# Kernel tuning notes

Measured on AMD Instinct MI355X. Metric: run time of the kernel, lower is better.

The kernel has to match this reference:

```python
import jax, jax.numpy as jnp
import numpy as np

NUM_HEADS = 12
HEAD_DIM = 64
HIDDEN = 768
SLOT_DIM = 30
BS = 8
FULL = SLOT_DIM * BS  # 240
SLOT_LEN = 32
LEN0 = 512   # slot-broadcast cache length
LEN1 = 128   # per-sample cache length


def tf_slot(x, slot_dim):
    # (slot_dim*bs, H, L, h) -> (bs, H, slot_dim*L, h)
    full, nh, L, h = x.shape
    bs = full // slot_dim
    x = x.reshape(slot_dim, bs, nh, L, h).transpose(1, 2, 0, 3, 4)
    return x.reshape(bs, nh, slot_dim * L, h)


def back_slot(x, slot_dim):
    # (bs, H, slot_dim*L, h) -> (slot_dim*bs, H, L, h)
    bs, nh, total, h = x.shape
    L = total // slot_dim
    x = x.reshape(bs, nh, slot_dim, L, h).transpose(2, 0, 1, 3, 4)
    return x.reshape(slot_dim * bs, nh, L, h)


def setup_inputs() -> dict:
    key = jax.random.key(0)
    ks = jax.random.split(key, 12)
    s = 0.02
    return {
        "hidden_states": jax.random.normal(ks[0], (FULL, SLOT_LEN, HIDDEN), jnp.float32),
        "attention_mask": jnp.zeros((FULL, 1, 1, LEN0 + LEN1 + SLOT_LEN), jnp.float32),
        "cache0_key": jax.random.normal(ks[1], (BS, NUM_HEADS, LEN0, HEAD_DIM), jnp.float32),
        "cache0_value": jax.random.normal(ks[2], (BS, NUM_HEADS, LEN0, HEAD_DIM), jnp.float32),
        "cache1_key": jax.random.normal(ks[3], (FULL, NUM_HEADS, LEN1, HEAD_DIM), jnp.float32),
        "cache1_value": jax.random.normal(ks[4], (FULL, NUM_HEADS, LEN1, HEAD_DIM), jnp.float32),
        "Wq": jax.random.normal(ks[5], (HIDDEN, HIDDEN), jnp.float32) * s,
        "bq": jax.random.normal(ks[6], (HIDDEN,), jnp.float32) * s,
        "Wk": jax.random.normal(ks[7], (HIDDEN, HIDDEN), jnp.float32) * s,
        "bk": jax.random.normal(ks[8], (HIDDEN,), jnp.float32) * s,
        "Wv": jax.random.normal(ks[9], (HIDDEN, HIDDEN), jnp.float32) * s,
        "bv": jax.random.normal(ks[10], (HIDDEN,), jnp.float32) * s,
        "slot_dim": SLOT_DIM,
    }


def reference(hidden_states, attention_mask, cache0_key, cache0_value,
              cache1_key, cache1_value, Wq, bq, Wk, bk, Wv, bv, slot_dim):
    B, L, hid = hidden_states.shape

    def split_heads(x):  # (B, L, hid) -> (B, H, L, h)
        return x.reshape(B, L, NUM_HEADS, HEAD_DIM).transpose(0, 2, 1, 3)

    q = split_heads(hidden_states @ Wq + bq)
    k = split_heads(hidden_states @ Wk + bk)
    v = split_heads(hidden_states @ Wv + bv)

    # self-attention scores (B, H, L, L)
    self_scores = jnp.einsum('bhqd,bhkd->bhqk', q, k)

    # cache0: slot-broadcast path (cache batch = bs, queries batch = slot_dim*bs)
    q_tf = tf_slot(q, slot_dim)  # (bs, H, slot_dim*L, h)
    s0 = back_slot(jnp.einsum('bhqd,bhkd->bhqk', q_tf, cache0_key), slot_dim)  # (B,H,L,LEN0)
    # cache1: direct path (matching batch)
    s1 = jnp.einsum('bhqd,bhkd->bhqk', q, cache1_key)  # (B,H,L,LEN1)

    scores = jnp.concatenate([s0, s1, self_scores], axis=-1)
    scores = scores / jnp.sqrt(jnp.float32(HEAD_DIM)) + attention_mask
    probs = jax.nn.softmax(scores, axis=-1)  # single softmax over all KV sources

    len0 = cache0_key.shape[2]
    len1 = cache1_key.shape[2]
    # self context
    ctx = jnp.einsum('bhqk,bhkd->bhqd', probs[..., -L:], v)
    # cache0 context via slot transform
    p0 = tf_slot(probs[..., :len0], slot_dim)  # (bs, H, slot_dim*L, LEN0)
    ctx = ctx + back_slot(jnp.einsum('bhqk,bhkd->bhqd', p0, cache0_value), slot_dim)
    # cache1 context direct
    ctx = ctx + jnp.einsum('bhqk,bhkd->bhqd', probs[..., len0:len0 + len1], cache1_value)

    # (B, H, L, h) -> (B, L, hid)
    return ctx.transpose(0, 2, 1, 3).reshape(B, L, hid)
```

## Files before the change

kernel.cpp:

```cpp
#include <hip/hip_runtime.h>
#include <math.h>

#define NUM_HEADS 12
#define HEAD_DIM  64
#define HIDDEN    768
#define BS        8
#define FULL      240
#define SLOT_LEN  32
#define LEN0      512
#define LEN1      128
#define KTOT      672
#define M_TOK     (FULL * SLOT_LEN)

typedef float f32x4 __attribute__((ext_vector_type(4)));
typedef short s16x8 __attribute__((ext_vector_type(8)));
typedef short s16x4 __attribute__((ext_vector_type(4)));

__device__ __forceinline__ short f2bf(float x) {
    unsigned u = __float_as_uint(x);
    unsigned r = (u + 0x7fffu + ((u >> 16) & 1u)) >> 16;
    return (short)r;
}

__device__ __forceinline__ void gll16(const short* g, short* l) {
    __builtin_amdgcn_global_load_lds(
        (const __attribute__((address_space(1))) unsigned int*)g,
        (__attribute__((address_space(3))) unsigned int*)l, 16, 0, 0);
}

__global__ __launch_bounds__(256) void cast_hs(const float* __restrict__ in,
                                               short* __restrict__ out, int n4) {
    int i = blockIdx.x * 256 + threadIdx.x;
    if (i < n4) {
        float4 v = ((const float4*)in)[i];
        s16x4 o = {f2bf(v.x), f2bf(v.y), f2bf(v.z), f2bf(v.w)};
        ((s16x4*)out)[i] = o;
    }
}

__global__ __launch_bounds__(256) void cast_k0(const float* __restrict__ k0,
                                               short* __restrict__ k0c) {
    const size_t base = (size_t)blockIdx.x * 2048;
    const int t = threadIdx.x;
    const int row = t >> 3, c8 = t & 7;
    const float* src = &k0[base + row * 64 + c8 * 8];
    float4 a = *(const float4*)src;
    float4 b = *(const float4*)(src + 4);
    s16x8 o = {f2bf(a.x), f2bf(a.y), f2bf(a.z), f2bf(a.w),
               f2bf(b.x), f2bf(b.y), f2bf(b.z), f2bf(b.w)};
    *(s16x8*)&k0c[base + row * 64 + (size_t)((c8 ^ (row & 7)) * 8)] = o;
}

__global__ __launch_bounds__(256) void trans_v0(const float* __restrict__ v0,
                                                short* __restrict__ v0t) {
    __shared__ float tile[32][65];
    const size_t base = (size_t)blockIdx.x * 2048;
    const int t = threadIdx.x;
#pragma unroll
    for (int i = 0; i < 2; ++i) {
        int f = t + i * 256;
        int kr = f >> 4, d4 = (f & 15) * 4;
        float4 v = *(const float4*)&v0[base + kr * 64 + d4];
        tile[kr][d4 + 0] = v.x; tile[kr][d4 + 1] = v.y;
        tile[kr][d4 + 2] = v.z; tile[kr][d4 + 3] = v.w;
    }
    __syncthreads();
#pragma unroll
    for (int i = 0; i < 2; ++i) {
        int g = t + i * 256;
        int d = g >> 3, kr4 = (g & 7) * 4;
        s16x4 o = {f2bf(tile[kr4 + 0][d]), f2bf(tile[kr4 + 1][d]),
                   f2bf(tile[kr4 + 2][d]), f2bf(tile[kr4 + 3][d])};
        int grp = (kr4 >> 3) ^ ((d >> 1) & 3);
        *(s16x4*)&v0t[base + d * 32 + grp * 8 + (kr4 & 7)] = o;
    }
}

__global__ __launch_bounds__(256) void cast_w_t(const float* __restrict__ Wq,
                                                const float* __restrict__ Wk,
                                                const float* __restrict__ Wv,
                                                short* __restrict__ WtAll) {
    const float* W = (blockIdx.z == 0) ? Wq : (blockIdx.z == 1) ? Wk : Wv;
    short* Wt = WtAll + (size_t)blockIdx.z * HIDDEN * HIDDEN;
    __shared__ __align__(16) float tile[32][33];
    const int kb0 = blockIdx.y * 32, nb0 = blockIdx.x * 32;
    const int r = threadIdx.x >> 3, c4 = (threadIdx.x & 7) * 4;
    float4 v = *(const float4*)&W[(size_t)(kb0 + r) * HIDDEN + nb0 + c4];
    tile[r][c4 + 0] = v.x; tile[r][c4 + 1] = v.y;
    tile[r][c4 + 2] = v.z; tile[r][c4 + 3] = v.w;
    __syncthreads();
    s16x4 o = {f2bf(tile[c4 + 0][r]), f2bf(tile[c4 + 1][r]),
               f2bf(tile[c4 + 2][r]), f2bf(tile[c4 + 3][r])};
    *(s16x4*)&Wt[(size_t)(nb0 + r) * HIDDEN + kb0 + c4] = o;
}

__global__ __launch_bounds__(256) void qkv_mfma(
    const short* __restrict__ hsb, const short* __restrict__ WtAll,
    const float* __restrict__ bq, const float* __restrict__ bk,
    const float* __restrict__ bv,
    short* __restrict__ qo, short* __restrict__ ko, short* __restrict__ vo)
{
    const int z = blockIdx.z;
    const short* Wt = WtAll + (size_t)z * HIDDEN * HIDDEN;
    const float* bias = (z == 0) ? bq : (z == 1) ? bk : bv;
    short* outp = (z == 0) ? qo : (z == 1) ? ko : vo;

    __shared__ __align__(16) short smem[128 * 128];
    short* As = smem;
    short* Bs = smem + 128 * 64;

    const int t = threadIdx.x;
    const int lane = t & 63, w = t >> 6;
    const int l15 = lane & 15, quad = lane >> 4;
    const int mBase = blockIdx.y * 128, nBase = blockIdx.x * 128;
    const int mw = (w & 1) * 64, nw = (w >> 1) * 64;

    const int srow_in = lane >> 3;
    const int scol8 = (lane & 7) ^ srow_in;

    f32x4 acc[4][4];
    const f32x4 z4 = {0.f, 0.f, 0.f, 0.f};
#pragma unroll
    for (int i = 0; i < 4; ++i)
#pragma unroll
        for (int j = 0; j < 4; ++j) acc[i][j] = z4;

    for (int kb = 0; kb < HIDDEN; kb += 64) {
        __syncthreads();
#pragma unroll
        for (int j = 0; j < 4; ++j) {
            int row = w * 32 + j * 8 + srow_in;
            gll16(&hsb[(size_t)(mBase + row) * HIDDEN + kb + scol8 * 8],
                  &As[(w * 32 + j * 8) * 64]);
            gll16(&Wt[(size_t)(nBase + row) * HIDDEN + kb + scol8 * 8],
                  &Bs[(w * 32 + j * 8) * 64]);
        }
        __syncthreads();
#pragma unroll
        for (int kc = 0; kc < 2; ++kc) {
            s16x8 a[4], b[4];
#pragma unroll
            for (int mt = 0; mt < 4; ++mt) {
                int row = mw + mt * 16 + l15;
                int c8 = (kc * 4 + quad) ^ (row & 7);
                a[mt] = *(const s16x8*)&As[row * 64 + c8 * 8];
            }
#pragma unroll
            for (int nt = 0; nt < 4; ++nt) {
                int row = nw + nt * 16 + l15;
                int c8 = (kc * 4 + quad) ^ (row & 7);
                b[nt] = *(const s16x8*)&Bs[row * 64 + c8 * 8];
            }
#pragma unroll
            for (int mt = 0; mt < 4; ++mt)
#pragma unroll
                for (int nt = 0; nt < 4; ++nt)
                    acc[mt][nt] = __builtin_amdgcn_mfma_f32_16x16x32_bf16(
                        a[mt], b[nt], acc[mt][nt], 0, 0, 0);
        }
    }

    __syncthreads();
#pragma unroll
    for (int nt = 0; nt < 4; ++nt) {
        float bvv = bias[nBase + nw + nt * 16 + l15];
        int col = nw + nt * 16 + l15;
#pragma unroll
        for (int mt = 0; mt < 4; ++mt)
#pragma unroll
            for (int r = 0; r < 4; ++r) {
                int row = mw + mt * 16 + quad * 4 + r;
                smem[row * 128 + col] = f2bf(acc[mt][nt][r] + bvv);
            }
    }
    __syncthreads();
#pragma unroll
    for (int i = 0; i < 8; ++i) {
        int f = t + i * 256;
        int row = f >> 4, c8 = (f & 15) * 8;
        uint4 val = *(const uint4*)&smem[row * 128 + c8];
        int m = mBase + row, n = nBase + c8;
        size_t dst = (((size_t)(m >> 5) * NUM_HEADS + (n >> 6)) * SLOT_LEN + (m & 31)) * 64 + (n & 63);
        *(uint4*)&outp[dst] = val;
    }
}

__global__ __launch_bounds__(256) void attn_mfma(
    const short* __restrict__ qb, const short* __restrict__ kbuf,
    const short* __restrict__ vbuf,
    const short* __restrict__ k0c, const short* __restrict__ v0t,
    const float* __restrict__ c1k, const float* __restrict__ c1v,
    const float* __restrict__ mask, float* __restrict__ out)
{
    __shared__ __align__(16) short Klds[4][32][64];
    __shared__ __align__(16) short Vt[4][64][32];
    __shared__ __align__(16) short Plds[4][32][32];

    const int t = threadIdx.x, lane = t & 63, w = t >> 6;
    const int task = blockIdx.x * 4 + w;
    const int B = task / 12, h = task % 12;
    const int l15 = lane & 15, quad = lane >> 4;

    const short* qp  = qb  + (size_t)(B * NUM_HEADS + h) * SLOT_LEN * 64;
    const short* ksp = kbuf + (size_t)(B * NUM_HEADS + h) * SLOT_LEN * 64;
    const short* vsp = vbuf + (size_t)(B * NUM_HEADS + h) * SLOT_LEN * 64;
    const short* k0p = k0c + (size_t)((B & 7) * NUM_HEADS + h) * LEN0 * 64;
    const short* v0p = v0t + (size_t)((B & 7) * NUM_HEADS + h) * LEN0 * 64;
    const float* k1p = c1k + (size_t)(B * NUM_HEADS + h) * LEN1 * 64;
    const float* v1p = c1v + (size_t)(B * NUM_HEADS + h) * LEN1 * 64;
    const float* mp  = mask + (size_t)B * KTOT;

    short (*K)[64] = Klds[w];
    short (*V)[32] = Vt[w];
    short (*P)[32] = Plds[w];
    short* Kf = &K[0][0];
    short* Vf = &V[0][0];

    const int skey = lane >> 4;
    const int sc4 = (lane & 15) << 2;

    s16x8 qf[2][2];
#pragma unroll
    for (int qh = 0; qh < 2; ++qh)
#pragma unroll
        for (int kc = 0; kc < 2; ++kc)
            qf[qh][kc] = *(const s16x8*)&qp[(qh * 16 + l15) * 64 + kc * 32 + quad * 8];

    const f32x4 z4 = {0.f, 0.f, 0.f, 0.f};
    f32x4 o[2][4];
    float lpart[2][4];
#pragma unroll
    for (int qh = 0; qh < 2; ++qh) {
#pragma unroll
        for (int dq = 0; dq < 4; ++dq) o[qh][dq] = z4;
#pragma unroll
        for (int r = 0; r < 4; ++r) lpart[qh][r] = 0.f;
    }

    s16x8 kpre[4], vpre[4];
    float4 kreg[8];
    float mreg0, mreg1;

    const float LOG2E = 1.4426950408889634f;
    const float SCL   = 0.125f * 1.4426950408889634f;

    auto issue_bf = [&](int c) {
        const short* kcb = k0p + c * 2048;
        const short* vcb = v0p + c * 2048;
#pragma unroll
        for (int i = 0; i < 4; ++i) {
            kpre[i] = *(const s16x8*)&kcb[(i * 64 + lane) * 8];
            vpre[i] = *(const s16x8*)&vcb[(i * 64 + lane) * 8];
        }
    };
    auto issue_k1 = [&](int c) {
        const float* sk = k1p + (c - 16) * 2048;
#pragma unroll
        for (int i = 0; i < 8; ++i)
            kreg[i] = *(const float4*)&sk[(i * 4 + skey) * 64 + sc4];
    };
    auto issue_mask = [&](int c) {
        mreg0 = mp[c * 32 + l15] * LOG2E;
        mreg1 = mp[c * 32 + 16 + l15] * LOG2E;
    };

    issue_bf(0);
    issue_mask(0);

    for (int c = 0; c < 21; ++c) {
        const float mv0 = mreg0, mv1 = mreg1;
        float4 vv[8];
        bool f32path = (c >= 16 && c < 20);

        if (c < 16) {
#pragma unroll
            for (int i = 0; i < 4; ++i)
                *(s16x8*)&Kf[(i * 64 + lane) * 8] = kpre[i];
#pragma unroll
            for (int i = 0; i < 4; ++i)
                *(s16x8*)&Vf[(i * 64 + lane) * 8] = vpre[i];
            if (c + 1 < 16) issue_bf(c + 1);
            if (c == 15) issue_k1(16);
        } else if (c < 20) {
#pragma unroll
            for (int i = 0; i < 8; ++i) {
                s16x4 kk = {f2bf(kreg[i].x), f2bf(kreg[i].y), f2bf(kreg[i].z), f2bf(kreg[i].w)};
                int row = i * 4 + skey;
                *(s16x4*)&K[row][((l15 >> 1) ^ (row & 7)) * 8 + (l15 & 1) * 4] = kk;
            }
            const float* sv = v1p + (c - 16) * 2048;
#pragma unroll
            for (int i = 0; i < 8; ++i)
                vv[i] = *(const float4*)&sv[(i * 4 + skey) * 64 + sc4];
            if (c + 1 < 20) issue_k1(c + 1);
        } else {
#pragma unroll
            for (int i = 0; i < 8; ++i) {
                int key = i * 4 + skey;
                *(s16x4*)&K[key][((l15 >> 1) ^ (key & 7)) * 8 + (l15 & 1) * 4] =
                    *(const s16x4*)&ksp[key * 64 + sc4];
            }
            short vtmp[32];
#pragma unroll
            for (int key = 0; key < 32; ++key) vtmp[key] = vsp[key * 64 + lane];
#pragma unroll
            for (int k4 = 0; k4 < 8; ++k4) {
                s16x4 vo4 = {vtmp[k4 * 4 + 0], vtmp[k4 * 4 + 1],
                             vtmp[k4 * 4 + 2], vtmp[k4 * 4 + 3]};
                int grp = (k4 >> 1) ^ ((lane >> 1) & 3);
                *(s16x4*)&V[lane][grp * 8 + (k4 & 1) * 4] = vo4;
            }
        }

        if (c + 1 < 21) issue_mask(c + 1);

        f32x4 s[2][2];
#pragma unroll
        for (int qh = 0; qh < 2; ++qh)
#pragma unroll
            for (int kh = 0; kh < 2; ++kh) s[qh][kh] = z4;
#pragma unroll
        for (int kh = 0; kh < 2; ++kh) {
            int rowk = kh * 16 + l15;
            s16x8 kf0 = *(const s16x8*)&K[rowk][(quad ^ (rowk & 7)) * 8];
            s16x8 kf1 = *(const s16x8*)&K[rowk][((4 + quad) ^ (rowk & 7)) * 8];
#pragma unroll
            for (int qh = 0; qh < 2; ++qh) {
                s[qh][kh] = __builtin_amdgcn_mfma_f32_16x16x32_bf16(qf[qh][0], kf0, s[qh][kh], 0, 0, 0);
                s[qh][kh] = __builtin_amdgcn_mfma_f32_16x16x32_bf16(qf[qh][1], kf1, s[qh][kh], 0, 0, 0);
            }
        }

#pragma unroll
        for (int qh = 0; qh < 2; ++qh)
#pragma unroll
            for (int kh = 0; kh < 2; ++kh) {
                float mv = kh ? mv1 : mv0;
#pragma unroll
                for (int r = 0; r < 4; ++r) {
                    float p = exp2f(fmaf(s[qh][kh][r], SCL, mv));
                    lpart[qh][r] += p;
                    int prow = qh * 16 + quad * 4 + r;
                    int pswz = ((kh * 2 + (l15 >> 3)) ^ ((prow >> 1) & 3)) * 8 + (l15 & 7);
                    P[prow][pswz] = f2bf(p);
                }
            }

        if (f32path) {
#pragma unroll
            for (int i = 0; i < 8; ++i) {
                int key = i * 4 + skey;
                int kg = key >> 3, ks = key & 7;
#pragma unroll
                for (int j = 0; j < 4; ++j) {
                    int rowv = sc4 + j;
                    float fv = (j == 0) ? vv[i].x : (j == 1) ? vv[i].y : (j == 2) ? vv[i].z : vv[i].w;
                    V[rowv][(kg ^ ((rowv >> 1) & 3)) * 8 + ks] = f2bf(fv);
                }
            }
        }

#pragma unroll
        for (int qh = 0; qh < 2; ++qh) {
            int prow2 = qh * 16 + l15;
            int pg = (quad ^ ((l15 >> 1) & 3)) * 8;
            s16x4 plo = *(const s16x4*)&P[prow2][pg];
            s16x4 phi = *(const s16x4*)&P[prow2][pg + 4];
            s16x8 pf = __builtin_shufflevector(plo, phi, 0, 1, 2, 3, 4, 5, 6, 7);
#pragma unroll
            for (int dq = 0; dq < 4; ++dq) {
                int vrow = dq * 16 + l15;
                s16x8 vf = *(const s16x8*)&V[vrow][(quad ^ ((l15 >> 1) & 3)) * 8];
                o[qh][dq] = __builtin_amdgcn_mfma_f32_16x16x32_bf16(pf, vf, o[qh][dq], 0, 0, 0);
            }
        }
    }

    float linv[2][4];
#pragma unroll
    for (int qh = 0; qh < 2; ++qh)
#pragma unroll
        for (int r = 0; r < 4; ++r) {
            float l = lpart[qh][r];
            l += __shfl_xor(l, 1);
            l += __shfl_xor(l, 2);
            l += __shfl_xor(l, 4);
            l += __shfl_xor(l, 8);
            linv[qh][r] = 1.f / l;
        }

#pragma unroll
    for (int qh = 0; qh < 2; ++qh)
#pragma unroll
        for (int dq = 0; dq < 4; ++dq)
#pragma unroll
            for (int r = 0; r < 4; ++r) {
                int row = qh * 16 + quad * 4 + r;
                out[((size_t)B * SLOT_LEN + row) * HIDDEN + h * 64 + dq * 16 + l15] =
                    o[qh][dq][r] * linv[qh][r];
            }
}

extern "C" void kernel_launch(void* const* d_in, const int* in_sizes, int n_in,
                              void* d_out, int out_size, void* d_ws, size_t ws_size,
                              hipStream_t stream) {
    const float* hs   = (const float*)d_in[0];
    const float* mask = (const float*)d_in[1];
    const float* c0k  = (const float*)d_in[2];
    const float* c0v  = (const float*)d_in[3];
    const float* c1k  = (const float*)d_in[4];
    const float* c1v  = (const float*)d_in[5];
    const float* Wq   = (const float*)d_in[6];
    const float* bq   = (const float*)d_in[7];
    const float* Wk   = (const float*)d_in[8];
    const float* bk   = (const float*)d_in[9];
    const float* Wv   = (const float*)d_in[10];
    const float* bv   = (const float*)d_in[11];
    float* out = (float*)d_out;

    short* hsb = (short*)d_ws;
    short* WtA = hsb + (size_t)M_TOK * HIDDEN;
    short* qb  = WtA + (size_t)3 * HIDDEN * HIDDEN;
    short* kbw = qb + (size_t)M_TOK * HIDDEN;
    short* vbw = kbw + (size_t)M_TOK * HIDDEN;
    short* k0c = (short*)d_ws;
    short* v0t = k0c + (size_t)BS * NUM_HEADS * LEN0 * HEAD_DIM;

    cast_hs<<<(M_TOK * HIDDEN / 4 + 255) / 256, 256, 0, stream>>>(hs, hsb, M_TOK * HIDDEN / 4);
    cast_w_t<<<dim3(24, 24, 3), 256, 0, stream>>>(Wq, Wk, Wv, WtA);
    qkv_mfma<<<dim3(HIDDEN / 128, M_TOK / 128, 3), 256, 0, stream>>>(
        hsb, WtA, bq, bk, bv, qb, kbw, vbw);
    cast_k0<<<BS * NUM_HEADS * (LEN0 / 32), 256, 0, stream>>>(c0k, k0c);
    trans_v0<<<BS * NUM_HEADS * (LEN0 / 32), 256, 0, stream>>>(c0v, v0t);
    attn_mfma<<<720, 256, 0, stream>>>(qb, kbw, vbw, k0c, v0t, c1k, c1v, mask, out);
}
```

Measured before the change: 407.8 us.

## Split each attention task's KV chunks across four waves and merge via LDS

The attention kernel now assigns one (batch, head) task per block instead of per wave. The four waves each process a disjoint subset of the KV chunks (four cache0 chunks, one cache1 chunk, plus the self chunk on wave 3), and the partial outputs and row sums are reduced through shared memory before a vectorized store. This quadruples the block count and shortens each wave's serial chunk loop. In exchange it adds block syncs, an LDS reduction pass and less intra-wave prefetch pipelining. The cast_k0 and trans_v0 prep kernels are also merged into one launch.

```diff
diff --git a/kernel.cpp b/kernel.cpp
--- a/kernel.cpp
+++ b/kernel.cpp
@@ -38,41 +38,40 @@
     }
 }
 
-__global__ __launch_bounds__(256) void cast_k0(const float* __restrict__ k0,
-                                               short* __restrict__ k0c) {
-    const size_t base = (size_t)blockIdx.x * 2048;
-    const int t = threadIdx.x;
-    const int row = t >> 3, c8 = t & 7;
-    const float* src = &k0[base + row * 64 + c8 * 8];
-    float4 a = *(const float4*)src;
-    float4 b = *(const float4*)(src + 4);
-    s16x8 o = {f2bf(a.x), f2bf(a.y), f2bf(a.z), f2bf(a.w),
-               f2bf(b.x), f2bf(b.y), f2bf(b.z), f2bf(b.w)};
-    *(s16x8*)&k0c[base + row * 64 + (size_t)((c8 ^ (row & 7)) * 8)] = o;
-}
-
-__global__ __launch_bounds__(256) void trans_v0(const float* __restrict__ v0,
-                                                short* __restrict__ v0t) {
+__global__ __launch_bounds__(256) void prep_c0(const float* __restrict__ k0,
+                                               const float* __restrict__ v0,
+                                               short* __restrict__ k0c,
+                                               short* __restrict__ v0t) {
     __shared__ float tile[32][65];
     const size_t base = (size_t)blockIdx.x * 2048;
     const int t = threadIdx.x;
-#pragma unroll
-    for (int i = 0; i < 2; ++i) {
-        int f = t + i * 256;
-        int kr = f >> 4, d4 = (f & 15) * 4;
-        float4 v = *(const float4*)&v0[base + kr * 64 + d4];
-        tile[kr][d4 + 0] = v.x; tile[kr][d4 + 1] = v.y;
-        tile[kr][d4 + 2] = v.z; tile[kr][d4 + 3] = v.w;
-    }
-    __syncthreads();
-#pragma unroll
-    for (int i = 0; i < 2; ++i) {
-        int g = t + i * 256;
-        int d = g >> 3, kr4 = (g & 7) * 4;
-        s16x4 o = {f2bf(tile[kr4 + 0][d]), f2bf(tile[kr4 + 1][d]),
-                   f2bf(tile[kr4 + 2][d]), f2bf(tile[kr4 + 3][d])};
-        int grp = (kr4 >> 3) ^ ((d >> 1) & 3);
-        *(s16x4*)&v0t[base + d * 32 + grp * 8 + (kr4 & 7)] = o;
+    if (blockIdx.y == 0) {
+        const int row = t >> 3, c8 = t & 7;
+        const float* src = &k0[base + row * 64 + c8 * 8];
+        float4 a = *(const float4*)src;
+        float4 b = *(const float4*)(src + 4);
+        s16x8 o = {f2bf(a.x), f2bf(a.y), f2bf(a.z), f2bf(a.w),
+                   f2bf(b.x), f2bf(b.y), f2bf(b.z), f2bf(b.w)};
+        *(s16x8*)&k0c[base + row * 64 + (size_t)((c8 ^ (row & 7)) * 8)] = o;
+    } else {
+#pragma unroll
+        for (int i = 0; i < 2; ++i) {
+            int f = t + i * 256;
+            int kr = f >> 4, d4 = (f & 15) * 4;
+            float4 v = *(const float4*)&v0[base + kr * 64 + d4];
+            tile[kr][d4 + 0] = v.x; tile[kr][d4 + 1] = v.y;
+            tile[kr][d4 + 2] = v.z; tile[kr][d4 + 3] = v.w;
+        }
+        __syncthreads();
+#pragma unroll
+        for (int i = 0; i < 2; ++i) {
+            int g = t + i * 256;
+            int d = g >> 3, kr4 = (g & 7) * 4;
+            s16x4 o = {f2bf(tile[kr4 + 0][d]), f2bf(tile[kr4 + 1][d]),
+                       f2bf(tile[kr4 + 2][d]), f2bf(tile[kr4 + 3][d])};
+            int grp = (kr4 >> 3) ^ ((d >> 1) & 3);
+            *(s16x4*)&v0t[base + d * 32 + grp * 8 + (kr4 & 7)] = o;
+        }
     }
 }
 
@@ -192,12 +191,10 @@
     const float* __restrict__ c1k, const float* __restrict__ c1v,
     const float* __restrict__ mask, float* __restrict__ out)
 {
-    __shared__ __align__(16) short Klds[4][32][64];
-    __shared__ __align__(16) short Vt[4][64][32];
-    __shared__ __align__(16) short Plds[4][32][32];
+    __shared__ __align__(16) short sm_s[20480];
 
     const int t = threadIdx.x, lane = t & 63, w = t >> 6;
-    const int task = blockIdx.x * 4 + w;
+    const int task = blockIdx.x;
     const int B = task / 12, h = task % 12;
     const int l15 = lane & 15, quad = lane >> 4;
 
@@ -210,14 +207,17 @@
     const float* v1p = c1v + (size_t)(B * NUM_HEADS + h) * LEN1 * 64;
     const float* mp  = mask + (size_t)B * KTOT;
 
-    short (*K)[64] = Klds[w];
-    short (*V)[32] = Vt[w];
-    short (*P)[32] = Plds[w];
-    short* Kf = &K[0][0];
-    short* Vf = &V[0][0];
+    short (*K)[64] = (short(*)[64])(sm_s + w * 5120);
+    short (*V)[32] = (short(*)[32])(sm_s + w * 5120 + 2048);
+    short (*P)[32] = (short(*)[32])(sm_s + w * 5120 + 4096);
+    short* Kf = sm_s + w * 5120;
+    short* Vf = sm_s + w * 5120 + 2048;
 
     const int skey = lane >> 4;
     const int sc4 = (lane & 15) << 2;
+
+    const float LOG2E = 1.4426950408889634f;
+    const float SCL   = 0.125f * 1.4426950408889634f;
 
     s16x8 qf[2][2];
 #pragma unroll
@@ -237,83 +237,7 @@
         for (int r = 0; r < 4; ++r) lpart[qh][r] = 0.f;
     }
 
-    s16x8 kpre[4], vpre[4];
-    float4 kreg[8];
-    float mreg0, mreg1;
-
-    const float LOG2E = 1.4426950408889634f;
-    const float SCL   = 0.125f * 1.4426950408889634f;
-
-    auto issue_bf = [&](int c) {
-        const short* kcb = k0p + c * 2048;
-        const short* vcb = v0p + c * 2048;
-#pragma unroll
-        for (int i = 0; i < 4; ++i) {
-            kpre[i] = *(const s16x8*)&kcb[(i * 64 + lane) * 8];
-            vpre[i] = *(const s16x8*)&vcb[(i * 64 + lane) * 8];
-        }
-    };
-    auto issue_k1 = [&](int c) {
-        const float* sk = k1p + (c - 16) * 2048;
-#pragma unroll
-        for (int i = 0; i < 8; ++i)
-            kreg[i] = *(const float4*)&sk[(i * 4 + skey) * 64 + sc4];
-    };
-    auto issue_mask = [&](int c) {
-        mreg0 = mp[c * 32 + l15] * LOG2E;
-        mreg1 = mp[c * 32 + 16 + l15] * LOG2E;
-    };
-
-    issue_bf(0);
-    issue_mask(0);
-
-    for (int c = 0; c < 21; ++c) {
-        const float mv0 = mreg0, mv1 = mreg1;
-        float4 vv[8];
-        bool f32path = (c >= 16 && c < 20);
-
-        if (c < 16) {
-#pragma unroll
-            for (int i = 0; i < 4; ++i)
-                *(s16x8*)&Kf[(i * 64 + lane) * 8] = kpre[i];
-#pragma unroll
-            for (int i = 0; i < 4; ++i)
-                *(s16x8*)&Vf[(i * 64 + lane) * 8] = vpre[i];
-            if (c + 1 < 16) issue_bf(c + 1);
-            if (c == 15) issue_k1(16);
-        } else if (c < 20) {
-#pragma unroll
-            for (int i = 0; i < 8; ++i) {
-                s16x4 kk = {f2bf(kreg[i].x), f2bf(kreg[i].y), f2bf(kreg[i].z), f2bf(kreg[i].w)};
-                int row = i * 4 + skey;
-                *(s16x4*)&K[row][((l15 >> 1) ^ (row & 7)) * 8 + (l15 & 1) * 4] = kk;
-            }
-            const float* sv = v1p + (c - 16) * 2048;
-#pragma unroll
-            for (int i = 0; i < 8; ++i)
-                vv[i] = *(const float4*)&sv[(i * 4 + skey) * 64 + sc4];
-            if (c + 1 < 20) issue_k1(c + 1);
-        } else {
-#pragma unroll
-            for (int i = 0; i < 8; ++i) {
-                int key = i * 4 + skey;
-                *(s16x4*)&K[key][((l15 >> 1) ^ (key & 7)) * 8 + (l15 & 1) * 4] =
-                    *(const s16x4*)&ksp[key * 64 + sc4];
-            }
-            short vtmp[32];
-#pragma unroll
-            for (int key = 0; key < 32; ++key) vtmp[key] = vsp[key * 64 + lane];
-#pragma unroll
-            for (int k4 = 0; k4 < 8; ++k4) {
-                s16x4 vo4 = {vtmp[k4 * 4 + 0], vtmp[k4 * 4 + 1],
-                             vtmp[k4 * 4 + 2], vtmp[k4 * 4 + 3]};
-                int grp = (k4 >> 1) ^ ((lane >> 1) & 3);
-                *(s16x4*)&V[lane][grp * 8 + (k4 & 1) * 4] = vo4;
-            }
-        }
-
-        if (c + 1 < 21) issue_mask(c + 1);
-
+    auto qk_exp = [&](float mv0, float mv1) {
         f32x4 s[2][2];
 #pragma unroll
         for (int qh = 0; qh < 2; ++qh)
@@ -330,7 +254,6 @@
                 s[qh][kh] = __builtin_amdgcn_mfma_f32_16x16x32_bf16(qf[qh][1], kf1, s[qh][kh], 0, 0, 0);
             }
         }
-
 #pragma unroll
         for (int qh = 0; qh < 2; ++qh)
 #pragma unroll
@@ -345,21 +268,8 @@
                     P[prow][pswz] = f2bf(p);
                 }
             }
-
-        if (f32path) {
-#pragma unroll
-            for (int i = 0; i < 8; ++i) {
-                int key = i * 4 + skey;
-                int kg = key >> 3, ks = key & 7;
-#pragma unroll
-                for (int j = 0; j < 4; ++j) {
-                    int rowv = sc4 + j;
-                    float fv = (j == 0) ? vv[i].x : (j == 1) ? vv[i].y : (j == 2) ? vv[i].z : vv[i].w;
-                    V[rowv][(kg ^ ((rowv >> 1) & 3)) * 8 + ks] = f2bf(fv);
-                }
-            }
-        }
-
+    };
+    auto pv = [&]() {
 #pragma unroll
         for (int qh = 0; qh < 2; ++qh) {
             int prow2 = qh * 16 + l15;
@@ -374,9 +284,119 @@
                 o[qh][dq] = __builtin_amdgcn_mfma_f32_16x16x32_bf16(pf, vf, o[qh][dq], 0, 0, 0);
             }
         }
-    }
-
-    float linv[2][4];
+    };
+
+    if (w == 3) {
+#pragma unroll
+        for (int i = 0; i < 8; ++i) {
+            int key = i * 4 + skey;
+            *(s16x4*)&K[key][((l15 >> 1) ^ (key & 7)) * 8 + (l15 & 1) * 4] =
+                *(const s16x4*)&ksp[key * 64 + sc4];
+        }
+        short vtmp[32];
+#pragma unroll
+        for (int key = 0; key < 32; ++key) vtmp[key] = vsp[key * 64 + lane];
+#pragma unroll
+        for (int k4 = 0; k4 < 8; ++k4) {
+            s16x4 vo4 = {vtmp[k4 * 4 + 0], vtmp[k4 * 4 + 1],
+                         vtmp[k4 * 4 + 2], vtmp[k4 * 4 + 3]};
+            int grp = (k4 >> 1) ^ ((lane >> 1) & 3);
+            *(s16x4*)&V[lane][grp * 8 + (k4 & 1) * 4] = vo4;
+        }
+        float mv0 = mp[20 * 32 + l15] * LOG2E;
+        float mv1 = mp[20 * 32 + 16 + l15] * LOG2E;
+        qk_exp(mv0, mv1);
+        pv();
+    }
+
+    {
+        int c = 16 + w;
+        const float* sk = k1p + (c - 16) * 2048;
+        const float* sv = v1p + (c - 16) * 2048;
+        float4 kr[4], vv[4];
+#pragma unroll
+        for (int i = 0; i < 4; ++i)
+            kr[i] = *(const float4*)&sk[(i * 4 + skey) * 64 + sc4];
+#pragma unroll
+        for (int i = 0; i < 4; ++i)
+            vv[i] = *(const float4*)&sv[(i * 4 + skey) * 64 + sc4];
+#pragma unroll
+        for (int i = 0; i < 4; ++i) {
+            s16x4 kk = {f2bf(kr[i].x), f2bf(kr[i].y), f2bf(kr[i].z), f2bf(kr[i].w)};
+            int row = i * 4 + skey;
+            *(s16x4*)&K[row][((l15 >> 1) ^ (row & 7)) * 8 + (l15 & 1) * 4] = kk;
+        }
+#pragma unroll
+        for (int i = 0; i < 4; ++i)
+            kr[i] = *(const float4*)&sk[((i + 4) * 4 + skey) * 64 + sc4];
+#pragma unroll
+        for (int i = 0; i < 4; ++i) {
+            s16x4 kk = {f2bf(kr[i].x), f2bf(kr[i].y), f2bf(kr[i].z), f2bf(kr[i].w)};
+            int row = (i + 4) * 4 + skey;
+            *(s16x4*)&K[row][((l15 >> 1) ^ (row & 7)) * 8 + (l15 & 1) * 4] = kk;
+        }
+        float mv0 = mp[c * 32 + l15] * LOG2E;
+        float mv1 = mp[c * 32 + 16 + l15] * LOG2E;
+        qk_exp(mv0, mv1);
+#pragma unroll
+        for (int i = 0; i < 4; ++i) {
+            int key = i * 4 + skey;
+            int kg = key >> 3, ks = key & 7;
+#pragma unroll
+            for (int j = 0; j < 4; ++j) {
+                int rowv = sc4 + j;
+                float fv = (j == 0) ? vv[i].x : (j == 1) ? vv[i].y : (j == 2) ? vv[i].z : vv[i].w;
+                V[rowv][(kg ^ ((rowv >> 1) & 3)) * 8 + ks] = f2bf(fv);
+            }
+        }
+#pragma unroll
+        for (int i = 0; i < 4; ++i)
+            vv[i] = *(const float4*)&sv[((i + 4) * 4 + skey) * 64 + sc4];
+#pragma unroll
+        for (int i = 0; i < 4; ++i) {
+            int key = (i + 4) * 4 + skey;
+            int kg = key >> 3, ks = key & 7;
+#pragma unroll
+            for (int j = 0; j < 4; ++j) {
+                int rowv = sc4 + j;
+                float fv = (j == 0) ? vv[i].x : (j == 1) ? vv[i].y : (j == 2) ? vv[i].z : vv[i].w;
+                V[rowv][(kg ^ ((rowv >> 1) & 3)) * 8 + ks] = f2bf(fv);
+            }
+        }
+        pv();
+    }
+
+    {
+        s16x8 kpre[4], vpre[4];
+        const int cbase = w * 4;
+        auto issue_bf = [&](int c) {
+            const short* kcb = k0p + c * 2048;
+            const short* vcb = v0p + c * 2048;
+#pragma unroll
+            for (int i = 0; i < 4; ++i) {
+                kpre[i] = *(const s16x8*)&kcb[(i * 64 + lane) * 8];
+                vpre[i] = *(const s16x8*)&vcb[(i * 64 + lane) * 8];
+            }
+        };
+        issue_bf(cbase);
+#pragma unroll
+        for (int j = 0; j < 4; ++j) {
+            int c = cbase + j;
+#pragma unroll
+            for (int i = 0; i < 4; ++i)
+                *(s16x8*)&Kf[(i * 64 + lane) * 8] = kpre[i];
+#pragma unroll
+            for (int i = 0; i < 4; ++i)
+                *(s16x8*)&Vf[(i * 64 + lane) * 8] = vpre[i];
+            if (j + 1 < 4) issue_bf(c + 1);
+            float mv0 = mp[c * 32 + l15] * LOG2E;
+            float mv1 = mp[c * 32 + 16 + l15] * LOG2E;
+            qk_exp(mv0, mv1);
+            pv();
+        }
+    }
+
+    float lred[2][4];
 #pragma unroll
     for (int qh = 0; qh < 2; ++qh)
 #pragma unroll
@@ -386,19 +406,51 @@
             l += __shfl_xor(l, 2);
             l += __shfl_xor(l, 4);
             l += __shfl_xor(l, 8);
-            linv[qh][r] = 1.f / l;
-        }
-
+            lred[qh][r] = l;
+        }
+
+    __syncthreads();
+    float* smf = (float*)sm_s;
 #pragma unroll
     for (int qh = 0; qh < 2; ++qh)
 #pragma unroll
         for (int dq = 0; dq < 4; ++dq)
 #pragma unroll
             for (int r = 0; r < 4; ++r) {
-                int row = qh * 16 + quad * 4 + r;
-                out[((size_t)B * SLOT_LEN + row) * HIDDEN + h * 64 + dq * 16 + l15] =
-                    o[qh][dq][r] * linv[qh][r];
-            }
+                int row = qh * 16 + quad * 4 + r, col = dq * 16 + l15;
+                smf[w * 2048 + row * 64 + col] = o[qh][dq][r];
+            }
+    if (l15 == 0) {
+#pragma unroll
+        for (int qh = 0; qh < 2; ++qh)
+#pragma unroll
+            for (int r = 0; r < 4; ++r)
+                smf[8192 + w * 32 + qh * 16 + quad * 4 + r] = lred[qh][r];
+    }
+    __syncthreads();
+
+    {
+        int row = t >> 3, c8 = (t & 7) * 8;
+        float lt = smf[8192 + row] + smf[8192 + 32 + row] +
+                   smf[8192 + 64 + row] + smf[8192 + 96 + row];
+        float inv = 1.f / lt;
+        float4 o0, o1;
+#pragma unroll
+        for (int j = 0; j < 4; ++j) {
+            int col = c8 + j;
+            o0[j] = (smf[row * 64 + col] + smf[2048 + row * 64 + col] +
+                     smf[4096 + row * 64 + col] + smf[6144 + row * 64 + col]) * inv;
+        }
+#pragma unroll
+        for (int j = 0; j < 4; ++j) {
+            int col = c8 + 4 + j;
+            o1[j] = (smf[row * 64 + col] + smf[2048 + row * 64 + col] +
+                     smf[4096 + row * 64 + col] + smf[6144 + row * 64 + col]) * inv;
+        }
+        float* op = &out[((size_t)B * SLOT_LEN + row) * HIDDEN + h * 64 + c8];
+        *(float4*)op = o0;
+        *(float4*)(op + 4) = o1;
+    }
 }
 
 extern "C" void kernel_launch(void* const* d_in, const int* in_sizes, int n_in,
@@ -430,7 +482,6 @@
     cast_w_t<<<dim3(24, 24, 3), 256, 0, stream>>>(Wq, Wk, Wv, WtA);
     qkv_mfma<<<dim3(HIDDEN / 128, M_TOK / 128, 3), 256, 0, stream>>>(
         hsb, WtA, bq, bk, bv, qb, kbw, vbw);
-    cast_k0<<<BS * NUM_HEADS * (LEN0 / 32), 256, 0, stream>>>(c0k, k0c);
-    trans_v0<<<BS * NUM_HEADS * (LEN0 / 32), 256, 0, stream>>>(c0v, v0t);
-    attn_mfma<<<720, 256, 0, stream>>>(qb, kbw, vbw, k0c, v0t, c1k, c1v, mask, out);
-}
+    prep_c0<<<dim3(BS * NUM_HEADS * (LEN0 / 32), 2), 256, 0, stream>>>(c0k, c0v, k0c, v0t);
+    attn_mfma<<<FULL * NUM_HEADS, 256, 0, stream>>>(qb, kbw, vbw, k0c, v0t, c1k, c1v, mask, out);
+}
```

Measured after the change: 369.3 us. 1.1x faster.
